# Kernel tuning notes

Measured on AMD Instinct MI355X. Metric: run time of the kernel, lower is better.

The kernel has to match this reference:

```python
import jax, jax.numpy as jnp
import numpy as np

N = 4096      # num_nodes
D_IN = 768    # input_dim
HID = 512     # hidden_dim per head
D_OUT = 768   # output_dim
H = 4         # num_heads
ALPHA = 0.2   # LeakyReLU slope
NEG_BIG = -9e15


def _layer_norm(x, g, b, eps=1e-5):
    m = jnp.mean(x, axis=-1, keepdims=True)
    v = jnp.var(x, axis=-1, keepdims=True)
    return (x - m) * jax.lax.rsqrt(v + eps) * g + b


def _multihead_gat(h, mask, ew, W, a, concat):
    # h: [N, F_in], W: [H, F_in, O], a: [H, 2*O], mask/ew: [N, N]
    O = W.shape[-1]
    Wh = jnp.einsum('nf,hfo->hno', h, W)                      # [H, N, O]
    # e[h,i,j] = leakyrelu(a1.Wh[i] + a2.Wh[j]) -- equivalent to the
    # concat(Wh_i, Wh_j) @ a formulation, without the O(N^2 * 2O) tensor.
    s_src = jnp.einsum('hno,ho->hn', Wh, a[:, :O])            # [H, N]
    s_dst = jnp.einsum('hno,ho->hn', Wh, a[:, O:])            # [H, N]
    e = jax.nn.leaky_relu(s_src[:, :, None] + s_dst[:, None, :], negative_slope=ALPHA)
    att = jnp.where(mask[None], e, NEG_BIG)
    if ew is not None:
        att = att * ew[None]                                   # faithful: scale AFTER masking
    att = jax.nn.softmax(att, axis=-1)                         # dropout is identity at eval
    hp = jnp.einsum('hnm,hmo->hno', att, Wh)                   # [H, N, O]
    if concat:
        return jax.nn.elu(jnp.transpose(hp, (1, 0, 2)).reshape(h.shape[0], H * O))
    return jnp.mean(hp, axis=0)                                # concat=False: mean, no ELU


def setup_inputs() -> dict:
    key = jax.random.key(0)
    ks = jax.random.split(key, 10)
    return {
        'node_features': jax.random.normal(ks[0], (N, D_IN), jnp.float32),
        'adjacency': jax.random.randint(ks[1], (N, N), 0, 2, jnp.int32),
        'edge_weights': jax.random.uniform(ks[2], (N, N), jnp.float32),
        'W0': (jax.random.normal(ks[3], (H, D_IN, HID)) * 0.05).astype(jnp.float32),
        'a0': (jax.random.normal(ks[4], (H, 2 * HID)) * 0.05).astype(jnp.float32),
        'W1': (jax.random.normal(ks[5], (H, HID * H, D_OUT)) * 0.02).astype(jnp.float32),
        'a1': (jax.random.normal(ks[6], (H, 2 * D_OUT)) * 0.05).astype(jnp.float32),
        'rp0_w': (jax.random.normal(ks[7], (D_IN, HID * H)) * 0.02).astype(jnp.float32),
        'rp0_b': jnp.zeros((HID * H,), jnp.float32),
        'rp1_w': (jax.random.normal(ks[8], (HID * H, D_OUT)) * 0.02).astype(jnp.float32),
        'rp1_b': jnp.zeros((D_OUT,), jnp.float32),
        'ln0_g': jnp.ones((HID * H,), jnp.float32),
        'ln0_b': jnp.zeros((HID * H,), jnp.float32),
        'ln1_g': jnp.ones((D_OUT,), jnp.float32),
        'ln1_b': jnp.zeros((D_OUT,), jnp.float32),
    }


def reference(node_features, adjacency, edge_weights, W0, a0, W1, a1,
              rp0_w, rp0_b, rp1_w, rp1_b, ln0_g, ln0_b, ln1_g, ln1_b):
    n = node_features.shape[0]
    adj = adjacency.astype(jnp.float32) + jnp.eye(n, dtype=jnp.float32)  # add self-loops
    mask = adj > 0
    h = node_features
    # layer 0: concat heads -> [N, H*HID], residual projection, LN, ELU (dropout=identity)
    h1 = _multihead_gat(h, mask, edge_weights, W0, a0, concat=True)
    h1 = h1 + (h @ rp0_w + rp0_b)
    h1 = _layer_norm(h1, ln0_g, ln0_b)
    h1 = jax.nn.elu(h1)
    # layer 1 (last): mean over heads -> [N, D_OUT], residual projection, LN
    h2 = _multihead_gat(h1, mask, edge_weights, W1, a1, concat=False)
    h2 = h2 + (h1 @ rp1_w + rp1_b)
    h2 = _layer_norm(h2, ln1_g, ln1_b)
    return h2
```

## Files before the change

### kernel.cpp

```cpp
#include <hip/hip_runtime.h>


typedef unsigned short u16;
typedef unsigned char u8;
typedef unsigned long long u64;
using short8  = __attribute__((ext_vector_type(8))) short;
using float4v = __attribute__((ext_vector_type(4))) float;
using int4v   = __attribute__((ext_vector_type(4))) int;
using int8v   = __attribute__((ext_vector_type(8))) int;

#define NN 4096
#define NHEADS 4

__device__ __forceinline__ u16 f2bf(float f) {
  union { float f; unsigned u; } v; v.f = f;
  unsigned u = v.u;
  return (u16)((u + 0x7FFFu + ((u >> 16) & 1u)) >> 16);
}
__device__ __forceinline__ float bf2f(u16 x) {
  union { unsigned u; float f; } v; v.u = ((unsigned)x) << 16; return v.f;
}
__device__ __forceinline__ unsigned pk_fp8x4(float a, float b, float c, float d) {
  int lo = __builtin_amdgcn_cvt_pk_fp8_f32(a, b, 0, false);
  return (unsigned)__builtin_amdgcn_cvt_pk_fp8_f32(c, d, lo, true);
}

__device__ __forceinline__ void async16(const void* g, void* l) {
  __builtin_amdgcn_global_load_lds(
      (const __attribute__((address_space(1))) unsigned int*)g,
      (__attribute__((address_space(3))) unsigned int*)l, 16, 0, 0);
}

__global__ __launch_bounds__(256) void cast_f32_bf16(const float* __restrict__ in,
                                                     u16* __restrict__ out, int n) {
  int i = blockIdx.x * 256 + threadIdx.x;
  if (i < n) out[i] = f2bf(in[i]);
}

__global__ __launch_bounds__(256) void adj2bits(const int* __restrict__ adj,
                                                u64* __restrict__ bits) {
  size_t gw = (size_t)blockIdx.x * 4 + (threadIdx.x >> 6);
  int lane = threadIdx.x & 63;
  int v = adj[gw * 64 + lane];
  u64 b = __ballot(v != 0);
  if (lane == 0) bits[gw] = b;
}

__global__ __launch_bounds__(256) void transcast_f32(const float* __restrict__ in,
                                                     u16* __restrict__ out, int R, int C) {
  __shared__ float t[32][33];
  size_t zoff = (size_t)blockIdx.z * R * C;
  in += zoff; out += zoff;
  int c0 = blockIdx.x * 32, r0 = blockIdx.y * 32;
  int tx = threadIdx.x & 31, ty = threadIdx.x >> 5;
#pragma unroll
  for (int i = 0; i < 32; i += 8)
    t[ty + i][tx] = in[(size_t)(r0 + ty + i) * C + (c0 + tx)];
  __syncthreads();
#pragma unroll
  for (int i = 0; i < 32; i += 8)
    out[(size_t)(c0 + ty + i) * R + (r0 + tx)] = f2bf(t[tx][ty + i]);
}

__global__ __launch_bounds__(256) void wa_kernel(const float* __restrict__ W,
                                                 const float* __restrict__ a,
                                                 float* __restrict__ wa, int F, int O) {
  int gw = blockIdx.x * 4 + (threadIdx.x >> 6);
  int lane = threadIdx.x & 63;
  int total = 2 * NHEADS * F;
  if (gw >= total) return;
  int side = gw / (NHEADS * F);
  int rem = gw - side * NHEADS * F;
  int h = rem / F, f = rem - h * F;
  const float* wrow = W + ((size_t)h * F + f) * O;
  const float* av = a + (size_t)h * 2 * O + (size_t)side * O;
  float s = 0.f;
  for (int o = lane; o < O; o += 64) s += wrow[o] * av[o];
#pragma unroll
  for (int off = 32; off > 0; off >>= 1) s += __shfl_down(s, off);
  if (lane == 0) wa[gw] = s;
}

__global__ __launch_bounds__(256) void s8_kernel_f32(const float* __restrict__ X,
                                                     const float* __restrict__ wa,
                                                     float* __restrict__ sout, int F) {
  int n = blockIdx.x * 4 + (threadIdx.x >> 6);
  int lane = threadIdx.x & 63;
  const float* x = X + (size_t)n * F;
  float acc[8] = {};
  for (int f = lane; f < F; f += 64) {
    float xv = x[f];
#pragma unroll
    for (int k = 0; k < 8; k++) acc[k] += xv * wa[(size_t)k * F + f];
  }
#pragma unroll
  for (int k = 0; k < 8; k++) {
    float s = acc[k];
#pragma unroll
    for (int off = 32; off > 0; off >>= 1) s += __shfl_down(s, off);
    if (lane == 0) sout[(size_t)k * NN + n] = s;
  }
}

__global__ __launch_bounds__(256) void s8_kernel_bf16(const u16* __restrict__ X,
                                                      const float* __restrict__ wa,
                                                      float* __restrict__ sout, int F) {
  int n = blockIdx.x * 4 + (threadIdx.x >> 6);
  int lane = threadIdx.x & 63;
  const u16* x = X + (size_t)n * F;
  float acc[8] = {};
  for (int f = lane; f < F; f += 64) {
    float xv = bf2f(x[f]);
#pragma unroll
    for (int k = 0; k < 8; k++) acc[k] += xv * wa[(size_t)k * F + f];
  }
#pragma unroll
  for (int k = 0; k < 8; k++) {
    float s = acc[k];
#pragma unroll
    for (int off = 32; off > 0; off >>= 1) s += __shfl_down(s, off);
    if (lane == 0) sout[(size_t)k * NN + n] = s;
  }
}

__global__ __launch_bounds__(256) void sdmax_kernel(const float* __restrict__ s,
                                                    float* __restrict__ out) {
  int h = blockIdx.x, tid = threadIdx.x;
  const float* sd = s + (size_t)(NHEADS + h) * NN;
  float m = -3e38f;
  for (int i = tid; i < NN; i += 256) m = fmaxf(m, sd[i]);
  __shared__ float red[4];
#pragma unroll
  for (int off = 32; off > 0; off >>= 1) m = fmaxf(m, __shfl_down(m, off));
  if ((tid & 63) == 0) red[tid >> 6] = m;
  __syncthreads();
  if (tid == 0) out[h] = fmaxf(fmaxf(red[0], red[1]), fmaxf(red[2], red[3]));
}

template <int G>
__global__ __launch_bounds__(256) void pexp_g_kernel(const u64* __restrict__ mb,
                                                     const float* __restrict__ ew,
                                                     const float* __restrict__ s,
                                                     const float* __restrict__ sdmax,
                                                     u8* __restrict__ P,
                                                     float* __restrict__ L, int hb) {
  __shared__ u64 mrow[64];
  __shared__ float lred[G][4];
  int i = blockIdx.x, tid = threadIdx.x;
  if (tid < 64) mrow[tid] = mb[(size_t)i * 64 + tid];
  float sr[G], mp[G], lacc[G];
#pragma unroll
  for (int z = 0; z < G; z++) {
    sr[z] = s[(size_t)(hb + z) * NN + i];
    mp[z] = fmaxf(0.0f, sr[z] + sdmax[hb + z]);
    lacc[z] = 0.f;
  }
  const float4* wrow = (const float4*)(ew + (size_t)i * NN);
  __syncthreads();
  for (int jv = tid; jv < NN / 4; jv += 256) {
    float4 w = wrow[jv];
    int j0 = jv * 4;
    u64 mw = mrow[jv >> 4] >> (j0 & 63);
    float we[4]; we[0] = w.x; we[1] = w.y; we[2] = w.z; we[3] = w.w;
    bool m[4];
#pragma unroll
    for (int k = 0; k < 4; k++) m[k] = ((mw >> k) & 1ull) || (j0 + k == i);
#pragma unroll
    for (int z = 0; z < G; z++) {
      const float4 sd4 = *(const float4*)(s + (size_t)(NHEADS + hb + z) * NN + j0);
      float sd[4]; sd[0] = sd4.x; sd[1] = sd4.y; sd[2] = sd4.z; sd[3] = sd4.w;
      float p[4];
#pragma unroll
      for (int k = 0; k < 4; k++) {
        float x = sr[z] + sd[k];
        float e = x > 0.f ? x : 0.2f * x;
        float v = (m[k] ? e : -9e15f) * we[k];
        p[k] = __expf(v - mp[z]);
        lacc[z] += p[k];
      }
      *(unsigned*)(P + ((size_t)z * NN + i) * NN + j0) = pk_fp8x4(p[0], p[1], p[2], p[3]);
    }
  }
#pragma unroll
  for (int z = 0; z < G; z++) {
    float r = lacc[z];
#pragma unroll
    for (int off = 32; off > 0; off >>= 1) r += __shfl_down(r, off);
    if ((tid & 63) == 0) lred[z][tid >> 6] = r;
  }
  __syncthreads();
  if (tid < G)
    L[(size_t)(hb + tid) * NN + i] = lred[tid][0] + lred[tid][1] + lred[tid][2] + lred[tid][3];
}

__global__ __launch_bounds__(256) void gemm_proj(const u16* __restrict__ A,
                                                 const u16* __restrict__ Bt,
                                                 u8* __restrict__ F8T,
                                                 float* __restrict__ F32,
                                                 const float* __restrict__ bias,
                                                 int K, int split, int ldcF) {
  int row0 = blockIdx.x * 128;
  int col0 = blockIdx.y * 128;

  __shared__ u16 ldsA[128 * 64];
  __shared__ u16 ldsB[128 * 64];

  int tid = threadIdx.x;
  int wave = tid >> 6, lane = tid & 63;
  int wm = wave >> 1, wn = wave & 1;
  int lm = lane & 15, quad = lane >> 4;

  int sr = tid >> 3, sc = tid & 7;
  int scg = sc ^ (sr & 7);
  const u16* aPtr = A  + (size_t)(row0 + sr) * K + scg * 8;
  const u16* bPtr = Bt + (size_t)(col0 + sr) * K + scg * 8;
  u16* ldsAw = &ldsA[wave * 512];
  u16* ldsBw = &ldsB[wave * 512];
  const size_t rowStep = (size_t)32 * K;

  float4v acc[4][4] = {};

  for (int k0 = 0; k0 < K; k0 += 64) {
    __syncthreads();
#pragma unroll
    for (int b = 0; b < 4; b++) {
      async16(aPtr + k0 + b * rowStep, ldsAw + b * 2048);
      async16(bPtr + k0 + b * rowStep, ldsBw + b * 2048);
    }
    __syncthreads();
    short8 af[4][2], bf[4][2];
#pragma unroll
    for (int s = 0; s < 4; s++) {
      int ra = wm * 64 + s * 16 + lm;
      int rb = wn * 64 + s * 16 + lm;
      int swa = ra & 7, swb = rb & 7;
      af[s][0] = *(const short8*)(&ldsA[ra * 64 + ((quad ^ swa) * 8)]);
      af[s][1] = *(const short8*)(&ldsA[ra * 64 + (((4 + quad) ^ swa) * 8)]);
      bf[s][0] = *(const short8*)(&ldsB[rb * 64 + ((quad ^ swb) * 8)]);
      bf[s][1] = *(const short8*)(&ldsB[rb * 64 + (((4 + quad) ^ swb) * 8)]);
    }
#pragma unroll
    for (int i = 0; i < 4; i++)
#pragma unroll
      for (int j = 0; j < 4; j++) {
        acc[i][j] = __builtin_amdgcn_mfma_f32_16x16x32_bf16(af[i][0], bf[j][0], acc[i][j], 0, 0, 0);
        acc[i][j] = __builtin_amdgcn_mfma_f32_16x16x32_bf16(af[i][1], bf[j][1], acc[i][j], 0, 0, 0);
      }
  }

  if (col0 < split) {
#pragma unroll
    for (int i = 0; i < 4; i++) {
#pragma unroll
      for (int j = 0; j < 4; j++) {
        int grow0 = row0 + wm * 64 + i * 16 + (lane >> 4) * 4;
        int gcol = col0 + wn * 64 + j * 16 + lm;
        unsigned pk = pk_fp8x4(acc[i][j][0], acc[i][j][1], acc[i][j][2], acc[i][j][3]);
        *(unsigned*)&F8T[(size_t)gcol * NN + grow0] = pk;
      }
    }
  } else {
#pragma unroll
    for (int i = 0; i < 4; i++) {
#pragma unroll
      for (int j = 0; j < 4; j++) {
#pragma unroll
        for (int r = 0; r < 4; r++) {
          int grow = row0 + wm * 64 + i * 16 + (lane >> 4) * 4 + r;
          int gcol = col0 + wn * 64 + j * 16 + lm - split;
          F32[(size_t)grow * ldcF + gcol] = acc[i][j][r] + bias[gcol];
        }
      }
    }
  }
}

template <int MODE>
__global__ __launch_bounds__(256) void gemm_mx(const u8* __restrict__ A,
                                               const u8* __restrict__ Bt,
                                               float* __restrict__ Cout,
                                               int ldc, int coloff_base, int coloff_step,
                                               size_t bStride, size_t cStride) {
  constexpr int K = NN;
  int h = blockIdx.z;
  const u8* Ab = A + (size_t)h * ((size_t)NN * NN);
  const u8* Bb = Bt + (size_t)h * bStride;
  int row0 = blockIdx.x * 128;
  int col0 = blockIdx.y * 128;
  int coloff = coloff_base + h * coloff_step;

  __shared__ u8 ldsA[128 * 128];
  __shared__ u8 ldsB[128 * 128];

  int tid = threadIdx.x;
  int wave = tid >> 6, lane = tid & 63;
  int wm = wave >> 1, wn = wave & 1;
  int lm = lane & 15, quad = lane >> 4;

  int sr = tid >> 3, sc = tid & 7;
  int scg = sc ^ (sr & 7);
  const u8* aPtr = Ab + (size_t)(row0 + sr) * K + scg * 16;
  const u8* bPtr = Bb + (size_t)(col0 + sr) * K + scg * 16;
  u8* ldsAw = &ldsA[wave * 1024];
  u8* ldsBw = &ldsB[wave * 1024];
  const size_t rowStep = (size_t)32 * K;

  float4v acc[4][4] = {};

  for (int k0 = 0; k0 < K; k0 += 128) {
    __syncthreads();
#pragma unroll
    for (int b = 0; b < 4; b++) {
      async16(aPtr + k0 + b * rowStep, ldsAw + b * 4096);
      async16(bPtr + k0 + b * rowStep, ldsBw + b * 4096);
    }
    __syncthreads();
    int8v a32[4], b32[4];
#pragma unroll
    for (int s = 0; s < 4; s++) {
      int ra = wm * 64 + s * 16 + lm;
      int rb = wn * 64 + s * 16 + lm;
      int swa = ra & 7, swb = rb & 7;
      int4v alo = *(const int4v*)(&ldsA[ra * 128 + (((2 * quad) ^ swa) * 16)]);
      int4v ahi = *(const int4v*)(&ldsA[ra * 128 + (((2 * quad + 1) ^ swa) * 16)]);
      int4v blo = *(const int4v*)(&ldsB[rb * 128 + (((2 * quad) ^ swb) * 16)]);
      int4v bhi = *(const int4v*)(&ldsB[rb * 128 + (((2 * quad + 1) ^ swb) * 16)]);
      a32[s][0] = alo[0]; a32[s][1] = alo[1]; a32[s][2] = alo[2]; a32[s][3] = alo[3];
      a32[s][4] = ahi[0]; a32[s][5] = ahi[1]; a32[s][6] = ahi[2]; a32[s][7] = ahi[3];
      b32[s][0] = blo[0]; b32[s][1] = blo[1]; b32[s][2] = blo[2]; b32[s][3] = blo[3];
      b32[s][4] = bhi[0]; b32[s][5] = bhi[1]; b32[s][6] = bhi[2]; b32[s][7] = bhi[3];
    }
#pragma unroll
    for (int i = 0; i < 4; i++)
#pragma unroll
      for (int j = 0; j < 4; j++)
        acc[i][j] = __builtin_amdgcn_mfma_scale_f32_16x16x128_f8f6f4(
            a32[i], b32[j], acc[i][j], 0, 0, 0, 127, 0, 127);
  }

#pragma unroll
  for (int i = 0; i < 4; i++) {
#pragma unroll
    for (int j = 0; j < 4; j++) {
#pragma unroll
      for (int r = 0; r < 4; r++) {
        int grow = row0 + wm * 64 + i * 16 + quad * 4 + r;
        int gcol = col0 + wn * 64 + j * 16 + lm;
        float v = acc[i][j][r];
        if constexpr (MODE == 2) {
          Cout[(size_t)grow * ldc + coloff + gcol] = v;
        } else {
          Cout[(size_t)h * cStride + (size_t)grow * ldc + gcol] = v;
        }
      }
    }
  }
}

__global__ __launch_bounds__(256) void ln0_kernel(const float* __restrict__ accin,
                                                  const float* __restrict__ rp,
                                                  const float* __restrict__ Lsum,
                                                  const float* __restrict__ g,
                                                  const float* __restrict__ b,
                                                  u16* __restrict__ h1b) {
  const int C = 2048;
  int n = blockIdx.x, tid = threadIdx.x;
  __shared__ float xs[2048];
  __shared__ float red[2][4];
  __shared__ float mrs[2];
  float linv[NHEADS];
#pragma unroll
  for (int h = 0; h < NHEADS; h++) linv[h] = 1.0f / Lsum[(size_t)h * NN + n];
  float sum = 0.f, sq = 0.f;
  const float* ar = accin + (size_t)n * C;
  const float* rr = rp + (size_t)n * C;
  for (int c = tid; c < C; c += 256) {
    float v = ar[c] * linv[c >> 9];
    v = v > 0.f ? v : (__expf(v) - 1.f);
    float x = v + rr[c];
    xs[c] = x; sum += x; sq += x * x;
  }
#pragma unroll
  for (int off = 32; off > 0; off >>= 1) { sum += __shfl_down(sum, off); sq += __shfl_down(sq, off); }
  if ((tid & 63) == 0) { red[0][tid >> 6] = sum; red[1][tid >> 6] = sq; }
  __syncthreads();
  if (tid == 0) {
    float s = red[0][0] + red[0][1] + red[0][2] + red[0][3];
    float q = red[1][0] + red[1][1] + red[1][2] + red[1][3];
    float mean = s / C, var = q / C - mean * mean;
    mrs[0] = mean; mrs[1] = rsqrtf(var + 1e-5f);
  }
  __syncthreads();
  float mean = mrs[0], rstd = mrs[1];
  for (int c = tid; c < C; c += 256) {
    float y = (xs[c] - mean) * rstd * g[c] + b[c];
    float z = y > 0.f ? y : (__expf(y) - 1.f);
    h1b[(size_t)n * C + c] = f2bf(z);
  }
}

__global__ __launch_bounds__(256) void ln1_kernel(const float* __restrict__ hp1,
                                                  const float* __restrict__ rp1,
                                                  const float* __restrict__ Lsum,
                                                  const float* __restrict__ g,
                                                  const float* __restrict__ b,
                                                  float* __restrict__ out) {
  const int C = 768;
  int n = blockIdx.x, tid = threadIdx.x;
  __shared__ float xs[768];
  __shared__ float red[2][4];
  __shared__ float mrs[2];
  float linv[NHEADS];
#pragma unroll
  for (int h = 0; h < NHEADS; h++) linv[h] = 0.25f / Lsum[(size_t)h * NN + n];
  float sum = 0.f, sq = 0.f;
  for (int c = tid; c < C; c += 256) {
    float x = hp1[((size_t)0 * NN + n) * C + c] * linv[0] +
              hp1[((size_t)1 * NN + n) * C + c] * linv[1] +
              hp1[((size_t)2 * NN + n) * C + c] * linv[2] +
              hp1[((size_t)3 * NN + n) * C + c] * linv[3];
    x += rp1[(size_t)n * C + c];
    xs[c] = x; sum += x; sq += x * x;
  }
#pragma unroll
  for (int off = 32; off > 0; off >>= 1) { sum += __shfl_down(sum, off); sq += __shfl_down(sq, off); }
  if ((tid & 63) == 0) { red[0][tid >> 6] = sum; red[1][tid >> 6] = sq; }
  __syncthreads();
  if (tid == 0) {
    float s = red[0][0] + red[0][1] + red[0][2] + red[0][3];
    float q = red[1][0] + red[1][1] + red[1][2] + red[1][3];
    float mean = s / C, var = q / C - mean * mean;
    mrs[0] = mean; mrs[1] = rsqrtf(var + 1e-5f);
  }
  __syncthreads();
  float mean = mrs[0], rstd = mrs[1];
  for (int c = tid; c < C; c += 256)
    out[(size_t)n * C + c] = (xs[c] - mean) * rstd * g[c] + b[c];
}

extern "C" void kernel_launch(void* const* d_in, const int* in_sizes, int n_in,
                              void* d_out, int out_size, void* d_ws, size_t ws_size,
                              hipStream_t stream) {
  (void)in_sizes; (void)n_in; (void)out_size;
  const float* X    = (const float*)d_in[0];
  const int*   adj  = (const int*)d_in[1];
  const float* ew   = (const float*)d_in[2];
  const float* W0   = (const float*)d_in[3];
  const float* a0   = (const float*)d_in[4];
  const float* W1   = (const float*)d_in[5];
  const float* a1   = (const float*)d_in[6];
  const float* rp0w = (const float*)d_in[7];
  const float* rp0b = (const float*)d_in[8];
  const float* rp1w = (const float*)d_in[9];
  const float* rp1b = (const float*)d_in[10];
  const float* ln0g = (const float*)d_in[11];
  const float* ln0b = (const float*)d_in[12];
  const float* ln1g = (const float*)d_in[13];
  const float* ln1b = (const float*)d_in[14];
  float* out = (float*)d_out;
  char* wsb = (char*)d_ws;

  constexpr size_t OFF_XBF   = 0;
  constexpr size_t OFF_W0T   = 6291456;
  constexpr size_t OFF_RP0WT = 9437184;
  constexpr size_t OFF_W1T   = 12582912;
  constexpr size_t OFF_RP1WT = 25165824;
  constexpr size_t OFF_WA0   = 28311552;
  constexpr size_t OFF_WA1   = 28336128;
  constexpr size_t OFF_S0    = 28401664;
  constexpr size_t OFF_S1    = 28532736;
  constexpr size_t OFF_L0    = 28664320;
  constexpr size_t OFF_L1    = 28729856;
  constexpr size_t OFF_H1B   = 28795392;
  constexpr size_t D         = 45572608;
  constexpr size_t PD        = D + 50331648;
  constexpr size_t PN        = (size_t)NN * NN;
  constexpr size_t OFF_HP1   = PD + 4 * PN;
  constexpr size_t OFF_MASK  = 213344768;
  constexpr size_t OFF_SM0   = 215441920;
  constexpr size_t OFF_SM1   = 215442176;

  u16*   XBF   = (u16*)(wsb + OFF_XBF);
  u16*   W0T   = (u16*)(wsb + OFF_W0T);
  u16*   RP0WT = (u16*)(wsb + OFF_RP0WT);
  u16*   W1T   = (u16*)(wsb + OFF_W1T);
  u16*   RP1WT = (u16*)(wsb + OFF_RP1WT);
  float* WA0   = (float*)(wsb + OFF_WA0);
  float* WA1   = (float*)(wsb + OFF_WA1);
  float* S0    = (float*)(wsb + OFF_S0);
  float* S1    = (float*)(wsb + OFF_S1);
  float* L0    = (float*)(wsb + OFF_L0);
  float* L1    = (float*)(wsb + OFF_L1);
  u16*   H1B   = (u16*)(wsb + OFF_H1B);
  u8*    WH0T  = (u8*)(wsb + D);
  float* RP0   = (float*)(wsb + D + 16777216);
  u8*    WH1T  = (u8*)(wsb + D);
  float* RP1   = (float*)(wsb + D + 25165824);
  u8*    P     = (u8*)(wsb + PD);
  float* HP1   = (float*)(wsb + OFF_HP1);
  float* ACC0  = (float*)(wsb + OFF_HP1);
  u64*   MASK  = (u64*)(wsb + OFF_MASK);
  float* SM0   = (float*)(wsb + OFF_SM0);
  float* SM1   = (float*)(wsb + OFF_SM1);

  const int G = (ws_size >= OFF_HP1 + 50331648) ? 4 : 1;

  adj2bits<<<dim3(65536), 256, 0, stream>>>(adj, MASK);
  cast_f32_bf16<<<dim3((NN * 768 + 255) / 256), 256, 0, stream>>>(X, XBF, NN * 768);
  transcast_f32<<<dim3(16, 24, 4), 256, 0, stream>>>(W0, W0T, 768, 512);
  transcast_f32<<<dim3(24, 64, 4), 256, 0, stream>>>(W1, W1T, 2048, 768);
  transcast_f32<<<dim3(64, 24, 1), 256, 0, stream>>>(rp0w, RP0WT, 768, 2048);
  transcast_f32<<<dim3(24, 64, 1), 256, 0, stream>>>(rp1w, RP1WT, 2048, 768);

  wa_kernel<<<dim3(2 * NHEADS * 768 / 4), 256, 0, stream>>>(W0, a0, WA0, 768, 512);
  s8_kernel_f32<<<dim3(NN / 4), 256, 0, stream>>>(X, WA0, S0, 768);
  sdmax_kernel<<<dim3(NHEADS), 256, 0, stream>>>(S0, SM0);

  gemm_proj<<<dim3(32, 32), 256, 0, stream>>>(XBF, W0T, WH0T, RP0, rp0b, 768, 2048, 2048);

  for (int g = 0; g < NHEADS; g += G) {
    if (G == 4) pexp_g_kernel<4><<<dim3(NN), 256, 0, stream>>>(MASK, ew, S0, SM0, P, L0, g);
    else        pexp_g_kernel<1><<<dim3(NN), 256, 0, stream>>>(MASK, ew, S0, SM0, P, L0, g);
    gemm_mx<2><<<dim3(32, 4, G), 256, 0, stream>>>(P, WH0T + (size_t)g * 512 * NN,
        ACC0, 2048, g * 512, 512, (size_t)512 * NN, 0);
  }
  ln0_kernel<<<dim3(NN), 256, 0, stream>>>(ACC0, RP0, L0, ln0g, ln0b, H1B);

  wa_kernel<<<dim3(2 * NHEADS * 2048 / 4), 256, 0, stream>>>(W1, a1, WA1, 2048, 768);
  s8_kernel_bf16<<<dim3(NN / 4), 256, 0, stream>>>(H1B, WA1, S1, 2048);
  sdmax_kernel<<<dim3(NHEADS), 256, 0, stream>>>(S1, SM1);

  gemm_proj<<<dim3(32, 30), 256, 0, stream>>>(H1B, W1T, WH1T, RP1, rp1b, 2048, 3072, 768);

  for (int g = 0; g < NHEADS; g += G) {
    if (G == 4) pexp_g_kernel<4><<<dim3(NN), 256, 0, stream>>>(MASK, ew, S1, SM1, P, L1, g);
    else        pexp_g_kernel<1><<<dim3(NN), 256, 0, stream>>>(MASK, ew, S1, SM1, P, L1, g);
    gemm_mx<3><<<dim3(32, 6, G), 256, 0, stream>>>(P, WH1T + (size_t)g * 768 * NN,
        HP1 + (size_t)g * NN * 768, 768, 0, 0, (size_t)768 * NN, (size_t)NN * 768);
  }
  ln1_kernel<<<dim3(NN), 256, 0, stream>>>(HP1, RP1, L1, ln1g, ln1b, out);
}
```

Before: 645.3 us.

## Double-buffer LDS tiles in projection and fp8 attention GEMMs with async prefetch

```diff
diff --git a/kernel.cpp b/kernel.cpp
--- a/kernel.cpp
+++ b/kernel.cpp
@@ -202,8 +202,8 @@
   int row0 = blockIdx.x * 128;
   int col0 = blockIdx.y * 128;
 
-  __shared__ u16 ldsA[128 * 64];
-  __shared__ u16 ldsB[128 * 64];
+  __shared__ u16 ldsA[2][128 * 64];
+  __shared__ u16 ldsB[2][128 * 64];
 
   int tid = threadIdx.x;
   int wave = tid >> 6, lane = tid & 63;
@@ -214,30 +214,41 @@
   int scg = sc ^ (sr & 7);
   const u16* aPtr = A  + (size_t)(row0 + sr) * K + scg * 8;
   const u16* bPtr = Bt + (size_t)(col0 + sr) * K + scg * 8;
-  u16* ldsAw = &ldsA[wave * 512];
-  u16* ldsBw = &ldsB[wave * 512];
   const size_t rowStep = (size_t)32 * K;
 
   float4v acc[4][4] = {};
 
-  for (int k0 = 0; k0 < K; k0 += 64) {
-    __syncthreads();
+  auto stage = [&](int buf, int k0) {
+    u16* la = &ldsA[buf][wave * 512];
+    u16* lb = &ldsB[buf][wave * 512];
 #pragma unroll
     for (int b = 0; b < 4; b++) {
-      async16(aPtr + k0 + b * rowStep, ldsAw + b * 2048);
-      async16(bPtr + k0 + b * rowStep, ldsBw + b * 2048);
-    }
-    __syncthreads();
+      async16(aPtr + k0 + b * rowStep, la + b * 2048);
+      async16(bPtr + k0 + b * rowStep, lb + b * 2048);
+    }
+  };
+
+  const int nt = K >> 6;
+  stage(0, 0);
+  stage(1, 64);
+  asm volatile("s_waitcnt vmcnt(8)" ::: "memory");
+  __builtin_amdgcn_s_barrier();
+  __builtin_amdgcn_sched_barrier(0);
+
+  for (int t = 0; t < nt; t++) {
+    int cur = t & 1;
+    const u16* LA = ldsA[cur];
+    const u16* LB = ldsB[cur];
     short8 af[4][2], bf[4][2];
 #pragma unroll
     for (int s = 0; s < 4; s++) {
       int ra = wm * 64 + s * 16 + lm;
       int rb = wn * 64 + s * 16 + lm;
       int swa = ra & 7, swb = rb & 7;
-      af[s][0] = *(const short8*)(&ldsA[ra * 64 + ((quad ^ swa) * 8)]);
-      af[s][1] = *(const short8*)(&ldsA[ra * 64 + (((4 + quad) ^ swa) * 8)]);
-      bf[s][0] = *(const short8*)(&ldsB[rb * 64 + ((quad ^ swb) * 8)]);
-      bf[s][1] = *(const short8*)(&ldsB[rb * 64 + (((4 + quad) ^ swb) * 8)]);
+      af[s][0] = *(const short8*)(&LA[ra * 64 + ((quad ^ swa) * 8)]);
+      af[s][1] = *(const short8*)(&LA[ra * 64 + (((4 + quad) ^ swa) * 8)]);
+      bf[s][0] = *(const short8*)(&LB[rb * 64 + ((quad ^ swb) * 8)]);
+      bf[s][1] = *(const short8*)(&LB[rb * 64 + (((4 + quad) ^ swb) * 8)]);
     }
 #pragma unroll
     for (int i = 0; i < 4; i++)
@@ -246,6 +257,16 @@
         acc[i][j] = __builtin_amdgcn_mfma_f32_16x16x32_bf16(af[i][0], bf[j][0], acc[i][j], 0, 0, 0);
         acc[i][j] = __builtin_amdgcn_mfma_f32_16x16x32_bf16(af[i][1], bf[j][1], acc[i][j], 0, 0, 0);
       }
+    __builtin_amdgcn_s_barrier();
+    __builtin_amdgcn_sched_barrier(0);
+    if (t + 2 < nt) {
+      stage(cur, (t + 2) << 6);
+      asm volatile("s_waitcnt vmcnt(8)" ::: "memory");
+    } else {
+      asm volatile("s_waitcnt vmcnt(0)" ::: "memory");
+    }
+    __builtin_amdgcn_s_barrier();
+    __builtin_amdgcn_sched_barrier(0);
   }
 
   if (col0 < split) {
@@ -289,8 +310,8 @@
   int col0 = blockIdx.y * 128;
   int coloff = coloff_base + h * coloff_step;
 
-  __shared__ u8 ldsA[128 * 128];
-  __shared__ u8 ldsB[128 * 128];
+  __shared__ u8 ldsA[2][128 * 128];
+  __shared__ u8 ldsB[2][128 * 128];
 
   int tid = threadIdx.x;
   int wave = tid >> 6, lane = tid & 63;
@@ -301,30 +322,41 @@
   int scg = sc ^ (sr & 7);
   const u8* aPtr = Ab + (size_t)(row0 + sr) * K + scg * 16;
   const u8* bPtr = Bb + (size_t)(col0 + sr) * K + scg * 16;
-  u8* ldsAw = &ldsA[wave * 1024];
-  u8* ldsBw = &ldsB[wave * 1024];
   const size_t rowStep = (size_t)32 * K;
 
   float4v acc[4][4] = {};
 
-  for (int k0 = 0; k0 < K; k0 += 128) {
-    __syncthreads();
+  auto stage = [&](int buf, int k0) {
+    u8* la = &ldsA[buf][wave * 1024];
+    u8* lb = &ldsB[buf][wave * 1024];
 #pragma unroll
     for (int b = 0; b < 4; b++) {
-      async16(aPtr + k0 + b * rowStep, ldsAw + b * 4096);
-      async16(bPtr + k0 + b * rowStep, ldsBw + b * 4096);
-    }
-    __syncthreads();
+      async16(aPtr + k0 + b * rowStep, la + b * 4096);
+      async16(bPtr + k0 + b * rowStep, lb + b * 4096);
+    }
+  };
+
+  const int nt = K >> 7;
+  stage(0, 0);
+  stage(1, 128);
+  asm volatile("s_waitcnt vmcnt(8)" ::: "memory");
+  __builtin_amdgcn_s_barrier();
+  __builtin_amdgcn_sched_barrier(0);
+
+  for (int t = 0; t < nt; t++) {
+    int cur = t & 1;
+    const u8* LA = ldsA[cur];
+    const u8* LB = ldsB[cur];
     int8v a32[4], b32[4];
 #pragma unroll
     for (int s = 0; s < 4; s++) {
       int ra = wm * 64 + s * 16 + lm;
       int rb = wn * 64 + s * 16 + lm;
       int swa = ra & 7, swb = rb & 7;
-      int4v alo = *(const int4v*)(&ldsA[ra * 128 + (((2 * quad) ^ swa) * 16)]);
-      int4v ahi = *(const int4v*)(&ldsA[ra * 128 + (((2 * quad + 1) ^ swa) * 16)]);
-      int4v blo = *(const int4v*)(&ldsB[rb * 128 + (((2 * quad) ^ swb) * 16)]);
-      int4v bhi = *(const int4v*)(&ldsB[rb * 128 + (((2 * quad + 1) ^ swb) * 16)]);
+      int4v alo = *(const int4v*)(&LA[ra * 128 + (((2 * quad) ^ swa) * 16)]);
+      int4v ahi = *(const int4v*)(&LA[ra * 128 + (((2 * quad + 1) ^ swa) * 16)]);
+      int4v blo = *(const int4v*)(&LB[rb * 128 + (((2 * quad) ^ swb) * 16)]);
+      int4v bhi = *(const int4v*)(&LB[rb * 128 + (((2 * quad + 1) ^ swb) * 16)]);
       a32[s][0] = alo[0]; a32[s][1] = alo[1]; a32[s][2] = alo[2]; a32[s][3] = alo[3];
       a32[s][4] = ahi[0]; a32[s][5] = ahi[1]; a32[s][6] = ahi[2]; a32[s][7] = ahi[3];
       b32[s][0] = blo[0]; b32[s][1] = blo[1]; b32[s][2] = blo[2]; b32[s][3] = blo[3];
@@ -336,6 +368,16 @@
       for (int j = 0; j < 4; j++)
         acc[i][j] = __builtin_amdgcn_mfma_scale_f32_16x16x128_f8f6f4(
             a32[i], b32[j], acc[i][j], 0, 0, 0, 127, 0, 127);
+    __builtin_amdgcn_s_barrier();
+    __builtin_amdgcn_sched_barrier(0);
+    if (t + 2 < nt) {
+      stage(cur, (t + 2) << 7);
+      asm volatile("s_waitcnt vmcnt(8)" ::: "memory");
+    } else {
+      asm volatile("s_waitcnt vmcnt(0)" ::: "memory");
+    }
+    __builtin_amdgcn_s_barrier();
+    __builtin_amdgcn_sched_barrier(0);
   }
 
 #pragma unroll
```

Result: faster. 604.3 us (-6.4%).
